# Kernel optimization log

Measured on AMD Instinct MI355X. Metric: run time of the kernel, lower is better.

## Reference

```python
import jax, jax.numpy as jnp
import numpy as np

B, S, D = 4, 1024, 1024
H, DK, DV = 16, 64, 64
EPS = 1e-6
NEG = -1e9


def setup_inputs() -> dict:
    key = jax.random.key(0)
    ks = jax.random.split(key, 8)
    scale = 0.02
    return {
        "q": jax.random.normal(ks[0], (B, S, D), jnp.float32),
        "k": jax.random.normal(ks[1], (B, S, D), jnp.float32),
        "v": jax.random.normal(ks[2], (B, S, D), jnp.float32),
        "mask": jax.random.randint(ks[3], (B, S, S), 0, 2, jnp.int32),
        # torch Linear(d_model, n_head*d_k, bias=False); stored here as [in, out]
        "w_qs": jax.random.normal(ks[4], (D, H * DK), jnp.float32) * scale,
        "w_ks": jax.random.normal(ks[5], (D, H * DK), jnp.float32) * scale,
        "w_vs": jax.random.normal(ks[6], (D, H * DV), jnp.float32) * scale,
        "w_fc": jax.random.normal(ks[7], (H * DV, D), jnp.float32) * scale,
        "ln_gamma": jnp.ones((D,), jnp.float32),
        "ln_beta": jnp.zeros((D,), jnp.float32),
    }


def reference(q, k, v, mask, w_qs, w_ks, w_vs, w_fc, ln_gamma, ln_beta):
    residual = q
    # projections -> (B, H, S, dk/dv)
    qh = (q @ w_qs).reshape(B, S, H, DK).transpose(0, 2, 1, 3)
    kh = (k @ w_ks).reshape(B, S, H, DK).transpose(0, 2, 1, 3)
    vh = (v @ w_vs).reshape(B, S, H, DV).transpose(0, 2, 1, 3)
    # scaled dot-product attention, mask broadcast over heads
    attn = jnp.einsum('bhqd,bhkd->bhqk', qh, kh) / jnp.sqrt(jnp.float32(DK))
    attn = jnp.where(mask[:, None, :, :] == 0, NEG, attn)
    attn = jax.nn.softmax(attn, axis=-1)  # dropout = identity at inference
    out = jnp.einsum('bhqk,bhkd->bhqd', attn, vh)
    out = out.transpose(0, 2, 1, 3).reshape(B, S, H * DV)
    out = out @ w_fc + residual
    # LayerNorm(eps=1e-6)
    mu = jnp.mean(out, axis=-1, keepdims=True)
    var = jnp.var(out, axis=-1, keepdims=True)
    out = (out - mu) / jnp.sqrt(var + EPS) * ln_gamma + ln_beta
    return out, attn
```

## Files before the change

kernel.cpp:

```cpp
#include <hip/hip_runtime.h>
#include <stdint.h>

typedef __bf16 bf16;
typedef __bf16 bf16x2 __attribute__((ext_vector_type(2)));
typedef __bf16 bf16x4 __attribute__((ext_vector_type(4)));
typedef __bf16 bf16x8 __attribute__((ext_vector_type(8)));
typedef float f32x4 __attribute__((ext_vector_type(4)));
typedef unsigned u32x2 __attribute__((ext_vector_type(2)));

__device__ __forceinline__ int swz(int row, int colb) {
    return (row * 64 + colb) ^ ((row & 7) << 4);
}

__device__ __forceinline__ unsigned packb(float a, float b) {
    bf16x2 t; t[0] = (bf16)a; t[1] = (bf16)b;
    return __builtin_bit_cast(unsigned, t);
}

__device__ __forceinline__ void gload16(void* lds, const void* g) {
    __builtin_amdgcn_global_load_lds(
        (const __attribute__((address_space(1))) void*)g,
        (__attribute__((address_space(3))) void*)lds, 16, 0, 0);
}

__global__ __launch_bounds__(256) void prep_kernel(
    const float* __restrict__ q, const float* __restrict__ k, const float* __restrict__ v,
    bf16* __restrict__ oq, bf16* __restrict__ ok, bf16* __restrict__ ov,
    const float* __restrict__ w0, const float* __restrict__ w1,
    const float* __restrict__ w2, const float* __restrict__ w3,
    bf16* __restrict__ t0, bf16* __restrict__ t1,
    bf16* __restrict__ t2, bf16* __restrict__ t3,
    const int* __restrict__ mask, unsigned long long* __restrict__ mbits)
{
    int bid = blockIdx.x;
    int tid = threadIdx.x;
    __shared__ float tile[32][33];

    if (bid < 6144) {
        int z = bid >> 11;
        int bx = bid & 2047;
        const float* src = z == 0 ? q : z == 1 ? k : v;
        bf16* dst = z == 0 ? oq : z == 1 ? ok : ov;
        size_t i = ((size_t)bx * 256 + tid) * 8;
        f32x4 a = *(const f32x4*)(src + i);
        f32x4 b = *(const f32x4*)(src + i + 4);
        bf16x8 o;
#pragma unroll
        for (int j = 0; j < 4; ++j) { o[j] = (bf16)a[j]; o[4 + j] = (bf16)b[j]; }
        *(bf16x8*)(dst + i) = o;
    } else if (bid < 10240) {
        int wid = bid - 6144;
        int z = wid >> 10;
        int t = wid & 1023;
        const float* W = z == 0 ? w0 : z == 1 ? w1 : z == 2 ? w2 : w3;
        bf16* O = z == 0 ? t0 : z == 1 ? t1 : z == 2 ? t2 : t3;
        int c0 = (t & 31) * 32, r0 = (t >> 5) * 32;
        int tx = tid & 31, ty = tid >> 5;
#pragma unroll
        for (int i = 0; i < 4; ++i)
            tile[ty + i * 8][tx] = W[(size_t)(r0 + ty + i * 8) * 1024 + c0 + tx];
        __syncthreads();
#pragma unroll
        for (int i = 0; i < 4; ++i)
            O[(size_t)(c0 + ty + i * 8) * 1024 + r0 + tx] = (bf16)tile[tx][ty + i * 8];
    } else {
        int mb = bid - 10240;
        int lane = tid & 63;
        int wid = (mb * 256 + tid) >> 6;
        int nw = (256 * 256) >> 6;
        const int niter = (4 * 1024 * 1024) / 64;
        for (int i = wid; i < niter; i += nw) {
            int vv = mask[(size_t)i * 64 + lane];
            unsigned long long bb = __ballot(vv != 0);
            if (lane == 0) mbits[i] = bb;
        }
    }
}

__global__ __launch_bounds__(256) void proj_gemm(
    const bf16* __restrict__ Aq, const bf16* __restrict__ Ak, const bf16* __restrict__ Av,
    const bf16* __restrict__ Wq, const bf16* __restrict__ Wk, const bf16* __restrict__ Wv,
    bf16* __restrict__ Oq, bf16* __restrict__ Ok, bf16* __restrict__ OvT)
{
    int z = blockIdx.z;
    const bf16* A = z == 0 ? Aq : z == 1 ? Ak : Av;
    const bf16* WT = z == 0 ? Wq : z == 1 ? Wk : Wv;

    __shared__ bf16 Al[128 * 32];
    __shared__ bf16 Bl[128 * 32];

    int tid = threadIdx.x;
    int w = tid >> 6, l = tid & 63;
    int l15 = l & 15, lg = l >> 4;
    int m0 = blockIdx.y * 128, n0 = blockIdx.x * 128;
    int wm = (w >> 1) * 64, wn = (w & 1) * 64;

    int rr0 = tid >> 2;
    int row0 = rr0 ^ ((rr0 >> 2) & 1);
    int cbe = (((tid & 3) * 16) ^ ((row0 & 3) << 4)) >> 1;
    char* aldst0 = (char*)Al + w * 1024;
    char* aldst1 = (char*)Al + 4096 + w * 1024;
    char* bldst0 = (char*)Bl + w * 1024;
    char* bldst1 = (char*)Bl + 4096 + w * 1024;
    const bf16* asrc0 = A + (size_t)(m0 + row0) * 1024 + cbe;
    const bf16* asrc1 = A + (size_t)(m0 + row0 + 64) * 1024 + cbe;
    const bf16* bsrc0 = WT + (size_t)(n0 + row0) * 1024 + cbe;
    const bf16* bsrc1 = WT + (size_t)(n0 + row0 + 64) * 1024 + cbe;

    const f32x4 fz = {0.f, 0.f, 0.f, 0.f};
    f32x4 acc[4][4];
#pragma unroll
    for (int i = 0; i < 4; ++i)
#pragma unroll
        for (int j = 0; j < 4; ++j) acc[i][j] = fz;

    for (int k0 = 0; k0 < 1024; k0 += 32) {
        gload16(aldst0, asrc0 + k0);
        gload16(aldst1, asrc1 + k0);
        gload16(bldst0, bsrc0 + k0);
        gload16(bldst1, bsrc1 + k0);
        __syncthreads();
        bf16x8 af[4], bv[4];
#pragma unroll
        for (int i = 0; i < 4; ++i)
            af[i] = *(const bf16x8*)((const char*)Al + swz(wm + i * 16 + l15, lg * 16));
#pragma unroll
        for (int j = 0; j < 4; ++j)
            bv[j] = *(const bf16x8*)((const char*)Bl + swz(wn + j * 16 + l15, lg * 16));
#pragma unroll
        for (int i = 0; i < 4; ++i)
#pragma unroll
            for (int j = 0; j < 4; ++j)
                acc[i][j] = __builtin_amdgcn_mfma_f32_16x16x32_bf16(af[i], bv[j], acc[i][j], 0, 0, 0);
        __syncthreads();
    }
    if (z < 2) {
        bf16* O = z == 0 ? Oq : Ok;
#pragma unroll
        for (int i = 0; i < 4; ++i)
#pragma unroll
            for (int j = 0; j < 4; ++j)
#pragma unroll
                for (int r = 0; r < 4; ++r) {
                    int m = m0 + wm + i * 16 + lg * 4 + r;
                    int n = n0 + wn + j * 16 + l15;
                    int bb = m >> 10, s = m & 1023, h = n >> 6, d = n & 63;
                    O[((size_t)(bb * 16 + h) * 1024 + s) * 64 + d] = (bf16)acc[i][j][r];
                }
    } else {
#pragma unroll
        for (int i = 0; i < 4; ++i)
#pragma unroll
            for (int j = 0; j < 4; ++j) {
                int m = m0 + wm + i * 16 + lg * 4;
                int n = n0 + wn + j * 16 + l15;
                int bb = m >> 10, s = m & 1023, h = n >> 6, d = n & 63;
                bf16x4 cv;
#pragma unroll
                for (int r = 0; r < 4; ++r) cv[r] = (bf16)acc[i][j][r];
                *(bf16x4*)(OvT + ((size_t)(bb * 16 + h) * 64 + d) * 1024 + s) = cv;
            }
    }
}

__global__ __launch_bounds__(256, 4) void attn_fused(
    const bf16* __restrict__ Qh, const bf16* __restrict__ Kh,
    const bf16* __restrict__ VhT, const unsigned* __restrict__ mbits,
    bf16* __restrict__ ctx, float* __restrict__ attn_out)
{
    int bh = blockIdx.x;
    int b = bh >> 4, h = bh & 15;
    int tid = threadIdx.x;
    int w = tid >> 6, l = tid & 63;
    int l15 = l & 15, lg = l >> 4;
    int q0 = blockIdx.y * 64 + w * 16;

    const bf16* Qb = Qh + (size_t)bh * 65536;
    const bf16* Kb = Kh + (size_t)bh * 65536;
    const bf16* Vt = VhT + (size_t)bh * 65536;
    const unsigned* mbrow = mbits + ((size_t)b * 1024 + q0 + l15) * 32;

    __shared__ char lds[26624];
    __shared__ float sinv[64];
    char* const Kl = lds;
    char* const Vl = lds + 8192;
    char* const St = lds + 16384 + w * 2048;
    char* const K0 = lds;
    char* const K1 = lds + 8192;
    char* const S2 = lds + 16384 + w * 2560;

    const int skr = tid >> 2;
    const int skb = (tid & 3) * 32;
    const int sks = (skr & 7) << 4;
    const int rsw = (l15 & 7) << 4;
    const int ko0 = (lg * 16) ^ rsw;
    const int ko1 = (64 + lg * 16) ^ rsw;

    bf16x8 qf0 = *(const bf16x8*)(Qb + (size_t)(q0 + l15) * 64 + lg * 8);
    bf16x8 qf1 = *(const bf16x8*)(Qb + (size_t)(q0 + l15) * 64 + 32 + lg * 8);

    const f32x4 fz = {0.f, 0.f, 0.f, 0.f};

    {
        const bf16* src = Kb + (size_t)skr * 64 + (skb >> 1);
        bf16x8 a = *(const bf16x8*)src;
        bf16x8 b2 = *(const bf16x8*)(src + 8);
        const bf16* vsrc = Vt + (size_t)skr * 1024 + (skb >> 1);
        bf16x8 va = *(const bf16x8*)vsrc;
        bf16x8 vb = *(const bf16x8*)(vsrc + 8);
        *(bf16x8*)(Kl + skr * 128 + (skb ^ sks)) = a;
        *(bf16x8*)(Kl + skr * 128 + ((skb + 16) ^ sks)) = b2;
        *(bf16x8*)(Vl + skr * 128 + (skb ^ sks)) = va;
        *(bf16x8*)(Vl + skr * 128 + ((skb + 16) ^ sks)) = vb;
    }
    __syncthreads();

    f32x4 oacc[4];
#pragma unroll
    for (int d0 = 0; d0 < 4; ++d0) oacc[d0] = fz;
    float ps = 0.f;

    for (int c = 0; c < 16; ++c) {
        bf16x8 nk0, nk1, nv0, nv1;
        if (c < 15) {
            const bf16* src = Kb + (size_t)((c + 1) * 64 + skr) * 64 + (skb >> 1);
            nk0 = *(const bf16x8*)src;
            nk1 = *(const bf16x8*)(src + 8);
            const bf16* vsrc = Vt + (size_t)skr * 1024 + (c + 1) * 64 + (skb >> 1);
            nv0 = *(const bf16x8*)vsrc;
            nv1 = *(const bf16x8*)(vsrc + 8);
        }
        u32x2 mw = *(const u32x2*)(mbrow + c * 2);
        f32x4 st[4];
#pragma unroll
        for (int f = 0; f < 4; ++f) st[f] = fz;
#pragma unroll
        for (int f = 0; f < 4; ++f) {
            bf16x8 kf = *(const bf16x8*)(Kl + (f * 16 + l15) * 128 + ko0);
            st[f] = __builtin_amdgcn_mfma_f32_16x16x32_bf16(kf, qf0, st[f], 0, 0, 0);
        }
#pragma unroll
        for (int f = 0; f < 4; ++f) {
            bf16x8 kf = *(const bf16x8*)(Kl + (f * 16 + l15) * 128 + ko1);
            st[f] = __builtin_amdgcn_mfma_f32_16x16x32_bf16(kf, qf1, st[f], 0, 0, 0);
        }
#pragma unroll
        for (int f = 0; f < 4; ++f) {
            unsigned wb = mw[f >> 1] >> (((f & 1) << 4) + (lg << 2));
            f32x4 o;
            o[0] = (wb & 1u)        ? __expf(st[f][0] * 0.125f) : 0.f;
            o[1] = ((wb >> 1) & 1u) ? __expf(st[f][1] * 0.125f) : 0.f;
            o[2] = ((wb >> 2) & 1u) ? __expf(st[f][2] * 0.125f) : 0.f;
            o[3] = ((wb >> 3) & 1u) ? __expf(st[f][3] * 0.125f) : 0.f;
            ps += (o[0] + o[1]) + (o[2] + o[3]);
            u32x2 pr; pr[0] = packb(o[0], o[1]); pr[1] = packb(o[2], o[3]);
            *(u32x2*)(St + l15 * 128 + ((f * 32 + lg * 8) ^ rsw)) = pr;
        }
#pragma unroll
        for (int ks = 0; ks < 2; ++ks) {
            bf16x8 pf = *(const bf16x8*)(St + l15 * 128 + ((ks * 64 + lg * 16) ^ rsw));
#pragma unroll
            for (int d0 = 0; d0 < 4; ++d0) {
                bf16x8 vf = *(const bf16x8*)(Vl + (d0 * 16 + l15) * 128 + ((ks * 64 + lg * 16) ^ rsw));
                oacc[d0] = __builtin_amdgcn_mfma_f32_16x16x32_bf16(vf, pf, oacc[d0], 0, 0, 0);
            }
        }
        __syncthreads();
        if (c < 15) {
            *(bf16x8*)(Kl + skr * 128 + (skb ^ sks)) = nk0;
            *(bf16x8*)(Kl + skr * 128 + ((skb + 16) ^ sks)) = nk1;
            *(bf16x8*)(Vl + skr * 128 + (skb ^ sks)) = nv0;
            *(bf16x8*)(Vl + skr * 128 + ((skb + 16) ^ sks)) = nv1;
        }
        __syncthreads();
    }
    ps += __shfl_xor(ps, 16, 64);
    ps += __shfl_xor(ps, 32, 64);
    float inv = 1.f / ps;
    if (l < 16) sinv[w * 16 + l15] = inv;

    bf16* crow = ctx + ((size_t)(b * 1024 + q0 + l15)) * 1024 + h * 64;
#pragma unroll
    for (int d0 = 0; d0 < 4; ++d0) {
        bf16x4 cv;
#pragma unroll
        for (int r = 0; r < 4; ++r) cv[r] = (bf16)(oacc[d0][r] * inv);
        *(bf16x4*)(crow + d0 * 16 + lg * 4) = cv;
    }
    __syncthreads();

    const int rq = l >> 3;
    const int rk = (l & 7) * 4;
    const float iv0 = sinv[w * 16 + rq];
    const float iv1 = sinv[w * 16 + 8 + rq];
    const unsigned* mb0 = mbits + ((size_t)b * 1024 + q0 + rq) * 32;
    const unsigned* mb1 = mbits + ((size_t)b * 1024 + q0 + 8 + rq) * 32;
    float* abase = attn_out + ((size_t)bh * 1024 + q0) * 1024;

    {
        const bf16* src = Kb + (size_t)skr * 64 + (skb >> 1);
        bf16x8 a = *(const bf16x8*)src;
        bf16x8 bb2 = *(const bf16x8*)(src + 8);
        *(bf16x8*)(K0 + skr * 128 + (skb ^ sks)) = a;
        *(bf16x8*)(K0 + skr * 128 + ((skb + 16) ^ sks)) = bb2;
    }

    for (int c = 0; c < 16; ++c) {
        __syncthreads();
        bf16x8 nk0, nk1;
        if (c < 15) {
            const bf16* src = Kb + (size_t)((c + 1) * 64 + skr) * 64 + (skb >> 1);
            nk0 = *(const bf16x8*)src;
            nk1 = *(const bf16x8*)(src + 8);
        }
        u32x2 mw0 = *(const u32x2*)(mb0 + c * 2);
        u32x2 mw1 = *(const u32x2*)(mb1 + c * 2);
        const char* Kc = (c & 1) ? K1 : K0;
        f32x4 st[4];
#pragma unroll
        for (int f = 0; f < 4; ++f) st[f] = fz;
#pragma unroll
        for (int f = 0; f < 4; ++f) {
            bf16x8 kf = *(const bf16x8*)(Kc + (f * 16 + l15) * 128 + ko0);
            st[f] = __builtin_amdgcn_mfma_f32_16x16x32_bf16(kf, qf0, st[f], 0, 0, 0);
        }
#pragma unroll
        for (int f = 0; f < 4; ++f) {
            bf16x8 kf = *(const bf16x8*)(Kc + (f * 16 + l15) * 128 + ko1);
            st[f] = __builtin_amdgcn_mfma_f32_16x16x32_bf16(kf, qf1, st[f], 0, 0, 0);
        }
        const int qsw = (l15 & 7) << 3;
#pragma unroll
        for (int f = 0; f < 4; ++f) {
#pragma unroll
            for (int j = 0; j < 2; ++j) {
                unsigned val = packb(__expf(st[f][2 * j] * 0.125f),
                                     __expf(st[f][2 * j + 1] * 0.125f));
                int kbyte = f * 32 + lg * 8 + j * 4;
                *(unsigned*)(S2 + l15 * 160 + (kbyte ^ qsw)) = val;
            }
        }
#pragma unroll
        for (int ri = 0; ri < 4; ++ri) {
            int qq = rq + 8 * (ri & 1);
            int kk = rk + 32 * (ri >> 1);
            bf16x4 pv4 = *(const bf16x4*)(S2 + qq * 160 + ((kk * 2) ^ ((qq & 7) << 3)));
            unsigned wm = ((ri & 1) ? mw1[ri >> 1] : mw0[ri >> 1]) >> rk;
            float iv = (ri & 1) ? iv1 : iv0;
            f32x4 o;
            o[0] = (wm & 1u)        ? (float)pv4[0] * iv : 0.f;
            o[1] = ((wm >> 1) & 1u) ? (float)pv4[1] * iv : 0.f;
            o[2] = ((wm >> 2) & 1u) ? (float)pv4[2] * iv : 0.f;
            o[3] = ((wm >> 3) & 1u) ? (float)pv4[3] * iv : 0.f;
            __builtin_nontemporal_store(o, (f32x4*)(abase + (size_t)qq * 1024 + c * 64 + kk));
        }
        if (c < 15) {
            char* kdst = ((c & 1) ? K0 : K1) + skr * 128;
            *(bf16x8*)(kdst + (skb ^ sks)) = nk0;
            *(bf16x8*)(kdst + ((skb + 16) ^ sks)) = nk1;
        }
    }
}

__global__ __launch_bounds__(256) void fc_gemm(
    const bf16* __restrict__ ctx, const bf16* __restrict__ WT,
    const float* __restrict__ resid, float* __restrict__ preLN)
{
    __shared__ bf16 Al[128 * 32];
    __shared__ bf16 Bl[128 * 32];
    int tid = threadIdx.x;
    int w = tid >> 6, l = tid & 63;
    int l15 = l & 15, lg = l >> 4;
    int m0 = blockIdx.y * 128, n0 = blockIdx.x * 128;
    int wm = (w >> 1) * 64, wn = (w & 1) * 64;

    int rr0 = tid >> 2;
    int row0 = rr0 ^ ((rr0 >> 2) & 1);
    int cbe = (((tid & 3) * 16) ^ ((row0 & 3) << 4)) >> 1;
    char* aldst0 = (char*)Al + w * 1024;
    char* aldst1 = (char*)Al + 4096 + w * 1024;
    char* bldst0 = (char*)Bl + w * 1024;
    char* bldst1 = (char*)Bl + 4096 + w * 1024;
    const bf16* asrc0 = ctx + (size_t)(m0 + row0) * 1024 + cbe;
    const bf16* asrc1 = ctx + (size_t)(m0 + row0 + 64) * 1024 + cbe;
    const bf16* bsrc0 = WT + (size_t)(n0 + row0) * 1024 + cbe;
    const bf16* bsrc1 = WT + (size_t)(n0 + row0 + 64) * 1024 + cbe;

    const f32x4 fz = {0.f, 0.f, 0.f, 0.f};
    f32x4 acc[4][4];
#pragma unroll
    for (int i = 0; i < 4; ++i)
#pragma unroll
        for (int j = 0; j < 4; ++j) acc[i][j] = fz;

    for (int k0 = 0; k0 < 1024; k0 += 32) {
        gload16(aldst0, asrc0 + k0);
        gload16(aldst1, asrc1 + k0);
        gload16(bldst0, bsrc0 + k0);
        gload16(bldst1, bsrc1 + k0);
        __syncthreads();
        bf16x8 af[4], bv[4];
#pragma unroll
    for (int i = 0; i < 4; ++i)
            af[i] = *(const bf16x8*)((const char*)Al + swz(wm + i * 16 + l15, lg * 16));
#pragma unroll
        for (int j = 0; j < 4; ++j)
            bv[j] = *(const bf16x8*)((const char*)Bl + swz(wn + j * 16 + l15, lg * 16));
#pragma unroll
        for (int i = 0; i < 4; ++i)
#pragma unroll
            for (int j = 0; j < 4; ++j)
                acc[i][j] = __builtin_amdgcn_mfma_f32_16x16x32_bf16(af[i], bv[j], acc[i][j], 0, 0, 0);
        __syncthreads();
    }
#pragma unroll
    for (int i = 0; i < 4; ++i)
#pragma unroll
        for (int j = 0; j < 4; ++j)
#pragma unroll
            for (int r = 0; r < 4; ++r) {
                int m = m0 + wm + i * 16 + lg * 4 + r;
                int n = n0 + wn + j * 16 + l15;
                preLN[(size_t)m * 1024 + n] = acc[i][j][r] + resid[(size_t)m * 1024 + n];
            }
}

__global__ __launch_bounds__(256) void ln_kernel(
    const float* __restrict__ x, const float* __restrict__ gamma,
    const float* __restrict__ beta, float* __restrict__ out)
{
    int row = blockIdx.x, t = threadIdx.x;
    const float* xr = x + (size_t)row * 1024;
    f32x4 v = *(const f32x4*)(xr + t * 4);
    float s = v[0] + v[1] + v[2] + v[3];
    float s2 = v[0] * v[0] + v[1] * v[1] + v[2] * v[2] + v[3] * v[3];
#pragma unroll
    for (int m = 1; m < 64; m <<= 1) {
        s += __shfl_xor(s, m, 64);
        s2 += __shfl_xor(s2, m, 64);
    }
    __shared__ float rs[4], rs2[4];
    if ((t & 63) == 0) { rs[t >> 6] = s; rs2[t >> 6] = s2; }
    __syncthreads();
    float S = rs[0] + rs[1] + rs[2] + rs[3];
    float S2 = rs2[0] + rs2[1] + rs2[2] + rs2[3];
    float mu = S * (1.f / 1024.f);
    float var = S2 * (1.f / 1024.f) - mu * mu;
    float rinv = rsqrtf(var + 1e-6f);
    f32x4 g = *(const f32x4*)(gamma + t * 4);
    f32x4 bb = *(const f32x4*)(beta + t * 4);
    f32x4 o;
#pragma unroll
    for (int j = 0; j < 4; ++j) o[j] = (v[j] - mu) * rinv * g[j] + bb[j];
    __builtin_nontemporal_store(o, (f32x4*)(out + (size_t)row * 1024 + t * 4));
}

extern "C" void kernel_launch(void* const* d_in, const int* in_sizes, int n_in,
                              void* d_out, int out_size, void* d_ws, size_t ws_size,
                              hipStream_t stream) {
    const float* q     = (const float*)d_in[0];
    const float* k     = (const float*)d_in[1];
    const float* v     = (const float*)d_in[2];
    const int*   mask  = (const int*)d_in[3];
    const float* w_qs  = (const float*)d_in[4];
    const float* w_ks  = (const float*)d_in[5];
    const float* w_vs  = (const float*)d_in[6];
    const float* w_fc  = (const float*)d_in[7];
    const float* gamma = (const float*)d_in[8];
    const float* beta  = (const float*)d_in[9];

    float* out  = (float*)d_out;
    float* attn = out + (size_t)4 * 1024 * 1024;

    char* ws = (char*)d_ws;
    bf16* wqT   = (bf16*)(ws + (0ull  << 20));
    bf16* wkT   = (bf16*)(ws + (2ull  << 20));
    bf16* wvT   = (bf16*)(ws + (4ull  << 20));
    bf16* wfcT  = (bf16*)(ws + (6ull  << 20));
    bf16* Qh    = (bf16*)(ws + (8ull  << 20));
    bf16* Kh    = (bf16*)(ws + (16ull << 20));
    bf16* VhT   = (bf16*)(ws + (32ull << 20));
    bf16* ctx   = (bf16*)(ws + (40ull << 20));
    float* preLN = (float*)(ws + (48ull << 20));
    unsigned long long* mbits = (unsigned long long*)(ws + (25ull << 20));

    char* scratch = (char*)attn;
    bf16* qb = (bf16*)scratch;
    bf16* kb = qb + (size_t)4 * 1024 * 1024;
    bf16* vb = kb + (size_t)4 * 1024 * 1024;

    prep_kernel<<<10496, 256, 0, stream>>>(q, k, v, qb, kb, vb,
                                           w_qs, w_ks, w_vs, w_fc,
                                           wqT, wkT, wvT, wfcT,
                                           mask, mbits);
    proj_gemm<<<dim3(8, 32, 3), 256, 0, stream>>>(qb, kb, vb, wqT, wkT, wvT,
                                                  Qh, Kh, VhT);
    attn_fused<<<dim3(64, 16), 256, 0, stream>>>(Qh, Kh, VhT, (const unsigned*)mbits,
                                                 ctx, attn);
    fc_gemm<<<dim3(8, 32), 256, 0, stream>>>(ctx, wfcT, q, preLN);
    ln_kernel<<<4096, 256, 0, stream>>>(preLN, gamma, beta, out);
}
```

Baseline: 193.0 us.

## Double-buffer K/V tiles in attention via direct global-to-LDS loads

Replaces the register-staged K and V tile loads in the fused attention kernel with global_load_lds direct-to-LDS transfers into double-buffered tiles. The next chunk is prefetched into the alternate buffer while the current one is consumed, which removes one of the two barriers per iteration in the first pass and the register round-trip for staging. LDS use grows from about 26 KB to 40 KB per block, which may reduce how many blocks fit per CU under the 4-block launch bound. The swizzle is now applied on the global source side to match the per-lane direct-load layout.

```diff
diff --git a/kernel.cpp b/kernel.cpp
--- a/kernel.cpp
+++ b/kernel.cpp
@@ -180,39 +180,37 @@
     const bf16* Vt = VhT + (size_t)bh * 65536;
     const unsigned* mbrow = mbits + ((size_t)b * 1024 + q0 + l15) * 32;
 
-    __shared__ char lds[26624];
-    __shared__ float sinv[64];
-    char* const Kl = lds;
-    char* const Vl = lds + 8192;
-    char* const St = lds + 16384 + w * 2048;
-    char* const K0 = lds;
-    char* const K1 = lds + 8192;
+    __shared__ char lds[40960];
+    char* const St = lds + 32768 + w * 2048;
+    float* const sinv = (float*)(lds + 32768);
     char* const S2 = lds + 16384 + w * 2560;
 
-    const int skr = tid >> 2;
-    const int skb = (tid & 3) * 32;
-    const int sks = (skr & 7) << 4;
     const int rsw = (l15 & 7) << 4;
     const int ko0 = (lg * 16) ^ rsw;
     const int ko1 = (64 + lg * 16) ^ rsw;
 
+    const int oA = (w * 2) * 1024 + l * 16;
+    const int oB = oA + 1024;
+    const int rA = oA >> 7, cA = oA & 127;
+    const int rB = oB >> 7, cB = oB & 127;
+    const int sAo = rA * 128 + (cA ^ ((rA & 7) << 4));
+    const int sBo = rB * 128 + (cB ^ ((rB & 7) << 4));
+    const int vAo = rA * 2048 + (cA ^ ((rA & 7) << 4));
+    const int vBo = rB * 2048 + (cB ^ ((rB & 7) << 4));
+    const char* KbS = (const char*)Kb;
+    const char* VtS = (const char*)Vt;
+    char* const kd = lds + (w * 2) * 1024;
+    char* const vd = lds + 16384 + (w * 2) * 1024;
+
     bf16x8 qf0 = *(const bf16x8*)(Qb + (size_t)(q0 + l15) * 64 + lg * 8);
     bf16x8 qf1 = *(const bf16x8*)(Qb + (size_t)(q0 + l15) * 64 + 32 + lg * 8);
 
     const f32x4 fz = {0.f, 0.f, 0.f, 0.f};
 
-    {
-        const bf16* src = Kb + (size_t)skr * 64 + (skb >> 1);
-        bf16x8 a = *(const bf16x8*)src;
-        bf16x8 b2 = *(const bf16x8*)(src + 8);
-        const bf16* vsrc = Vt + (size_t)skr * 1024 + (skb >> 1);
-        bf16x8 va = *(const bf16x8*)vsrc;
-        bf16x8 vb = *(const bf16x8*)(vsrc + 8);
-        *(bf16x8*)(Kl + skr * 128 + (skb ^ sks)) = a;
-        *(bf16x8*)(Kl + skr * 128 + ((skb + 16) ^ sks)) = b2;
-        *(bf16x8*)(Vl + skr * 128 + (skb ^ sks)) = va;
-        *(bf16x8*)(Vl + skr * 128 + ((skb + 16) ^ sks)) = vb;
-    }
+    gload16(kd,        KbS + sAo);
+    gload16(kd + 1024, KbS + sBo);
+    gload16(vd,        VtS + vAo);
+    gload16(vd + 1024, VtS + vBo);
     __syncthreads();
 
     f32x4 oacc[4];
@@ -221,27 +219,27 @@
     float ps = 0.f;
 
     for (int c = 0; c < 16; ++c) {
-        bf16x8 nk0, nk1, nv0, nv1;
         if (c < 15) {
-            const bf16* src = Kb + (size_t)((c + 1) * 64 + skr) * 64 + (skb >> 1);
-            nk0 = *(const bf16x8*)src;
-            nk1 = *(const bf16x8*)(src + 8);
-            const bf16* vsrc = Vt + (size_t)skr * 1024 + (c + 1) * 64 + (skb >> 1);
-            nv0 = *(const bf16x8*)vsrc;
-            nv1 = *(const bf16x8*)(vsrc + 8);
-        }
+            int nb = (c + 1) & 1;
+            gload16(kd + nb * 8192,        KbS + (c + 1) * 8192 + sAo);
+            gload16(kd + nb * 8192 + 1024, KbS + (c + 1) * 8192 + sBo);
+            gload16(vd + nb * 8192,        VtS + (c + 1) * 128 + vAo);
+            gload16(vd + nb * 8192 + 1024, VtS + (c + 1) * 128 + vBo);
+        }
+        const char* Kc = lds + (c & 1) * 8192;
+        const char* Vc = lds + 16384 + (c & 1) * 8192;
         u32x2 mw = *(const u32x2*)(mbrow + c * 2);
         f32x4 st[4];
 #pragma unroll
         for (int f = 0; f < 4; ++f) st[f] = fz;
 #pragma unroll
         for (int f = 0; f < 4; ++f) {
-            bf16x8 kf = *(const bf16x8*)(Kl + (f * 16 + l15) * 128 + ko0);
+            bf16x8 kf = *(const bf16x8*)(Kc + (f * 16 + l15) * 128 + ko0);
             st[f] = __builtin_amdgcn_mfma_f32_16x16x32_bf16(kf, qf0, st[f], 0, 0, 0);
         }
 #pragma unroll
         for (int f = 0; f < 4; ++f) {
-            bf16x8 kf = *(const bf16x8*)(Kl + (f * 16 + l15) * 128 + ko1);
+            bf16x8 kf = *(const bf16x8*)(Kc + (f * 16 + l15) * 128 + ko1);
             st[f] = __builtin_amdgcn_mfma_f32_16x16x32_bf16(kf, qf1, st[f], 0, 0, 0);
         }
 #pragma unroll
@@ -261,23 +259,15 @@
             bf16x8 pf = *(const bf16x8*)(St + l15 * 128 + ((ks * 64 + lg * 16) ^ rsw));
 #pragma unroll
             for (int d0 = 0; d0 < 4; ++d0) {
-                bf16x8 vf = *(const bf16x8*)(Vl + (d0 * 16 + l15) * 128 + ((ks * 64 + lg * 16) ^ rsw));
+                bf16x8 vf = *(const bf16x8*)(Vc + (d0 * 16 + l15) * 128 + ((ks * 64 + lg * 16) ^ rsw));
                 oacc[d0] = __builtin_amdgcn_mfma_f32_16x16x32_bf16(vf, pf, oacc[d0], 0, 0, 0);
             }
-        }
-        __syncthreads();
-        if (c < 15) {
-            *(bf16x8*)(Kl + skr * 128 + (skb ^ sks)) = nk0;
-            *(bf16x8*)(Kl + skr * 128 + ((skb + 16) ^ sks)) = nk1;
-            *(bf16x8*)(Vl + skr * 128 + (skb ^ sks)) = nv0;
-            *(bf16x8*)(Vl + skr * 128 + ((skb + 16) ^ sks)) = nv1;
         }
         __syncthreads();
     }
     ps += __shfl_xor(ps, 16, 64);
     ps += __shfl_xor(ps, 32, 64);
     float inv = 1.f / ps;
-    if (l < 16) sinv[w * 16 + l15] = inv;
 
     bf16* crow = ctx + ((size_t)(b * 1024 + q0 + l15)) * 1024 + h * 64;
 #pragma unroll
@@ -287,6 +277,8 @@
         for (int r = 0; r < 4; ++r) cv[r] = (bf16)(oacc[d0][r] * inv);
         *(bf16x4*)(crow + d0 * 16 + lg * 4) = cv;
     }
+    __syncthreads();
+    if (l < 16) sinv[w * 16 + l15] = inv;
     __syncthreads();
 
     const int rq = l >> 3;
@@ -297,25 +289,19 @@
     const unsigned* mb1 = mbits + ((size_t)b * 1024 + q0 + 8 + rq) * 32;
     float* abase = attn_out + ((size_t)bh * 1024 + q0) * 1024;
 
-    {
-        const bf16* src = Kb + (size_t)skr * 64 + (skb >> 1);
-        bf16x8 a = *(const bf16x8*)src;
-        bf16x8 bb2 = *(const bf16x8*)(src + 8);
-        *(bf16x8*)(K0 + skr * 128 + (skb ^ sks)) = a;
-        *(bf16x8*)(K0 + skr * 128 + ((skb + 16) ^ sks)) = bb2;
-    }
+    gload16(kd,        KbS + sAo);
+    gload16(kd + 1024, KbS + sBo);
 
     for (int c = 0; c < 16; ++c) {
         __syncthreads();
-        bf16x8 nk0, nk1;
         if (c < 15) {
-            const bf16* src = Kb + (size_t)((c + 1) * 64 + skr) * 64 + (skb >> 1);
-            nk0 = *(const bf16x8*)src;
-            nk1 = *(const bf16x8*)(src + 8);
+            int nb = (c + 1) & 1;
+            gload16(kd + nb * 8192,        KbS + (c + 1) * 8192 + sAo);
+            gload16(kd + nb * 8192 + 1024, KbS + (c + 1) * 8192 + sBo);
         }
         u32x2 mw0 = *(const u32x2*)(mb0 + c * 2);
         u32x2 mw1 = *(const u32x2*)(mb1 + c * 2);
-        const char* Kc = (c & 1) ? K1 : K0;
+        const char* Kc = lds + (c & 1) * 8192;
         f32x4 st[4];
 #pragma unroll
         for (int f = 0; f < 4; ++f) st[f] = fz;
@@ -354,11 +340,6 @@
             o[3] = ((wm >> 3) & 1u) ? (float)pv4[3] * iv : 0.f;
             __builtin_nontemporal_store(o, (f32x4*)(abase + (size_t)qq * 1024 + c * 64 + kk));
         }
-        if (c < 15) {
-            char* kdst = ((c & 1) ? K0 : K1) + skr * 128;
-            *(bf16x8*)(kdst + (skb ^ sks)) = nk0;
-            *(bf16x8*)(kdst + ((skb + 16) ^ sks)) = nk1;
-        }
     }
 }
 
@@ -401,7 +382,7 @@
         __syncthreads();
         bf16x8 af[4], bv[4];
 #pragma unroll
-    for (int i = 0; i < 4; ++i)
+        for (int i = 0; i < 4; ++i)
             af[i] = *(const bf16x8*)((const char*)Al + swz(wm + i * 16 + l15, lg * 16));
 #pragma unroll
         for (int j = 0; j < 4; ++j)
```

Result: no change. 196.5 us (+1.8%).
